# Performance work log

Measured on AMD Instinct MI355X. Metric: run time of the kernel, lower is better.

The kernel has to match this reference:

```python
import jax, jax.numpy as jnp
import numpy as np

N, E, D, L, G, T = 50000, 600000, 128, 4, 512, 10
EPS = 1e-5


def setup_inputs() -> dict:
    key = jax.random.key(0)
    ks = jax.random.split(key, 20)
    s = lambda k, shp, fan: jax.random.normal(k, shp, jnp.float32) * (1.0 / np.sqrt(fan))
    inp = {
        'x': jax.random.normal(ks[0], (N, 3), jnp.float32),
        'edge_index': jax.random.randint(ks[1], (2, E), 0, N, jnp.int32),
        'batch': jnp.sort(jax.random.randint(ks[2], (N,), 0, G, jnp.int32)),
        'emb_W': s(ks[3], (3, D), 3),
        'emb_b': jnp.zeros((D,), jnp.float32),
        'conv_W': s(ks[4], (L, 12 * D, D), 12 * D),
        'conv_b': jnp.zeros((L, D), jnp.float32),
        'bn_gamma': jnp.ones((L, D), jnp.float32),
        'bn_beta': jnp.zeros((L, D), jnp.float32),
        'W1': s(ks[5], (D, D // 2), D), 'b1': jnp.zeros((D // 2,), jnp.float32),
        'W2': s(ks[6], (D // 2, D // 4), D // 2), 'b2': jnp.zeros((D // 4,), jnp.float32),
        'W3': s(ks[7], (D // 4, T), D // 4), 'b3': jnp.zeros((T,), jnp.float32),
    }
    return inp


def reference(x, edge_index, batch, emb_W, emb_b, conv_W, conv_b, bn_gamma, bn_beta,
              W1, b1, W2, b2, W3, b3):
    n = x.shape[0]
    src, dst = edge_index[0], edge_index[1]  # messages flow src(j) -> dst(i)
    deg = jax.ops.segment_sum(jnp.ones((src.shape[0],), x.dtype), dst, num_segments=n)
    delta = jnp.mean(jnp.log1p(deg))          # avg log-degree (PNA's avg_deg['log'])
    d = jnp.maximum(deg, 1.0)[:, None]        # clamp(min=1)
    log_d = jnp.log1p(d)
    amp, att = log_d / delta, delta / log_d   # amplification / attenuation scalers
    has_edge = (deg > 0)[:, None]

    h = x @ emb_W + emb_b                     # node_emb Linear(3, D)
    for l in range(conv_W.shape[0]):
        msg = h[src]                          # [E, D] gather
        s1 = jax.ops.segment_sum(msg, dst, num_segments=n)
        s2 = jax.ops.segment_sum(msg * msg, dst, num_segments=n)
        mean = s1 / d
        std = jnp.sqrt(jax.nn.relu(s2 / d - mean * mean) + EPS)
        mn = jnp.where(has_edge, jax.ops.segment_min(msg, dst, num_segments=n), 0.0)
        mx = jnp.where(has_edge, jax.ops.segment_max(msg, dst, num_segments=n), 0.0)
        aggs = jnp.concatenate([mean, mn, mx, std], axis=-1)                 # [N, 4D]
        out = jnp.concatenate([aggs, aggs * amp, aggs * att], axis=-1)       # [N, 12D]
        out = out @ conv_W[l] + conv_b[l]      # post_nn Linear(12D, D)
        mu = out.mean(axis=0)
        var = out.var(axis=0)
        out = (out - mu) * jax.lax.rsqrt(var + EPS) * bn_gamma[l] + bn_beta[l]
        h = jax.nn.relu(out) + h               # residual (dropout off: eval)

    # global_mean_pool over graphs
    gsum = jax.ops.segment_sum(h, batch, num_segments=G)
    cnt = jnp.maximum(jax.ops.segment_sum(jnp.ones((n,), h.dtype), batch, num_segments=G), 1.0)
    g = gsum / cnt[:, None]
    g = jax.nn.relu(g @ W1 + b1)
    g = jax.nn.relu(g @ W2 + b2)
    return g @ W3 + b3                         # source='image': no clamp
```

## Files before the change

kernel.cpp:

```cpp
#include <hip/hip_runtime.h>
#include <math.h>

#define NN 50000
#define NE 600000
#define DD 128
#define NL 4
#define NG 512
#define NT 10
#define NPAD 50176
#define EPSF 1e-5f

typedef __bf16 bf16x8 __attribute__((ext_vector_type(8)));
typedef float f32x4 __attribute__((ext_vector_type(4)));

__device__ __forceinline__ unsigned short f2bf(float x) {
    union { float f; unsigned u; } v; v.f = x;
    unsigned r = v.u + 0x7FFFu + ((v.u >> 16) & 1u);
    return (unsigned short)(r >> 16);
}
__device__ __forceinline__ unsigned pack_bf2(float a, float b) {
    return (unsigned)f2bf(a) | ((unsigned)f2bf(b) << 16);
}
__device__ __forceinline__ float bf_lo(unsigned v) {
    union { unsigned u; float f; } w; w.u = (v & 0xFFFFu) << 16; return w.f;
}
__device__ __forceinline__ float bf_hi(unsigned v) {
    union { unsigned u; float f; } w; w.u = v & 0xFFFF0000u; return w.f;
}

__global__ void k_count(const int* __restrict__ dst, int* __restrict__ deg,
                        float* __restrict__ dsum, int E) {
    int e = blockIdx.x * blockDim.x + threadIdx.x;
    if (e == 0) *dsum = 0.f;
    if (e < E) atomicAdd(&deg[dst[e]], 1);
}

__global__ void k_scan_part(const int* __restrict__ deg, int* __restrict__ part, int n) {
    __shared__ int sm[256];
    int b = blockIdx.x, t = threadIdx.x;
    int base = b * 1024 + t * 4;
    int s = 0;
    #pragma unroll
    for (int j = 0; j < 4; j++) if (base + j < n) s += deg[base + j];
    sm[t] = s;
    __syncthreads();
    for (int off = 128; off > 0; off >>= 1) {
        if (t < off) sm[t] += sm[t + off];
        __syncthreads();
    }
    if (t == 0) part[b] = sm[0];
}

__global__ void k_scan_top(const int* __restrict__ part, int* __restrict__ offs,
                           int* __restrict__ row_ptr, int nb, int n) {
    if (threadIdx.x == 0) {
        int acc = 0;
        for (int i = 0; i < nb; i++) { offs[i] = acc; acc += part[i]; }
        row_ptr[n] = acc;
    }
}

__global__ void k_scan_apply(const int* __restrict__ deg, const int* __restrict__ offs,
                             int* __restrict__ row_ptr, int* __restrict__ cursor, int n) {
    __shared__ int sm[256];
    int b = blockIdx.x, t = threadIdx.x;
    int base = b * 1024 + t * 4;
    int v[4]; int s = 0;
    #pragma unroll
    for (int j = 0; j < 4; j++) { v[j] = (base + j < n) ? deg[base + j] : 0; s += v[j]; }
    sm[t] = s;
    __syncthreads();
    for (int off = 1; off < 256; off <<= 1) {
        int y = (t >= off) ? sm[t - off] : 0;
        __syncthreads();
        sm[t] += y;
        __syncthreads();
    }
    int run = offs[b] + sm[t] - s;
    #pragma unroll
    for (int j = 0; j < 4; j++) {
        if (base + j < n) { row_ptr[base + j] = run; cursor[base + j] = run; run += v[j]; }
    }
}

__global__ void k_fill(const int* __restrict__ src, const int* __restrict__ dst,
                       int* __restrict__ cursor, int* __restrict__ csr_src, int E) {
    int e = blockIdx.x * blockDim.x + threadIdx.x;
    if (e < E) {
        int d = dst[e];
        int pos = atomicAdd(&cursor[d], 1);
        csr_src[pos] = src[e];
    }
}

__global__ void k_delta(const int* __restrict__ deg, float* __restrict__ dsum, int n) {
    int i = blockIdx.x * blockDim.x + threadIdx.x;
    float v = (i < n) ? log1pf((float)deg[i]) : 0.f;
    #pragma unroll
    for (int off = 32; off > 0; off >>= 1) v += __shfl_down(v, off);
    if ((threadIdx.x & 63) == 0) atomicAdd(dsum, v);
}

__global__ void k_scalars(const int* __restrict__ deg, const float* __restrict__ dsum,
                          float* __restrict__ inv_d, float* __restrict__ amp,
                          float* __restrict__ att, int n) {
    int i = blockIdx.x * blockDim.x + threadIdx.x;
    if (i >= n) return;
    float delta = *dsum / (float)n;
    float d = fmaxf((float)deg[i], 1.f);
    float ld = log1pf(d);
    inv_d[i] = 1.f / d;
    amp[i] = ld / delta;
    att[i] = delta / ld;
}

__global__ void k_emb(const float* __restrict__ x, const float* __restrict__ W,
                      const float* __restrict__ b, float* __restrict__ h,
                      unsigned* __restrict__ hb2, int total2) {
    int i = blockIdx.x * blockDim.x + threadIdx.x;
    if (i >= total2) return;
    int node = i >> 6, c = (i & 63) * 2;
    float x0 = x[node * 3 + 0], x1 = x[node * 3 + 1], x2 = x[node * 3 + 2];
    float v0 = x0 * W[c] + x1 * W[DD + c] + x2 * W[2 * DD + c] + b[c];
    float v1 = x0 * W[c + 1] + x1 * W[DD + c + 1] + x2 * W[2 * DD + c + 1] + b[c + 1];
    ((float2*)h)[i] = make_float2(v0, v1);
    hb2[i] = pack_bf2(v0, v1);
}

__global__ void k_wconv(const float* __restrict__ W, unsigned short* __restrict__ Bt2, int total) {
    int o = blockIdx.x * blockDim.x + threadIdx.x;
    if (o >= total) return;
    int l = o / 196608;
    int idx = o % 196608;
    int kc = idx / 3072;
    int rem = idx % 3072;
    int j = rem >> 10;
    int nn = (rem >> 3) & 127;
    int k8 = rem & 7;
    int k = kc * 8 + k8;
    Bt2[o] = f2bf(W[(size_t)l * 196608 + (size_t)(j * 512 + k) * 128 + nn]);
}

__global__ void k_agg(const unsigned* __restrict__ hb2, const int* __restrict__ row_ptr,
                      const int* __restrict__ csr_src, const float* __restrict__ inv_d,
                      unsigned* __restrict__ atw, float* __restrict__ bn_zero) {
    __shared__ unsigned ldsb[16 * 260];
    int tid = threadIdx.x;
    if (blockIdx.x == 0) bn_zero[tid] = 0.f;
    int w = tid >> 6, t = tid & 63;
    int node0 = blockIdx.x * 16;
    #pragma unroll 1
    for (int q = 0; q < 4; q++) {
        int nl = w * 4 + q;
        int node = node0 + nl;
        int beg = row_ptr[node], end = row_ptr[node + 1];
        float s1a = 0.f, s1b = 0.f, s2a = 0.f, s2b = 0.f;
        float mna = INFINITY, mnb = INFINITY, mxa = -INFINITY, mxb = -INFINITY;
        int e = beg;
        for (; e + 1 < end; e += 2) {
            int sa = csr_src[e], sb = csr_src[e + 1];
            unsigned va = hb2[(size_t)sa * 64 + t];
            unsigned vb = hb2[(size_t)sb * 64 + t];
            float a0 = bf_lo(va), b0 = bf_hi(va);
            float a1 = bf_lo(vb), b1 = bf_hi(vb);
            s1a += a0 + a1; s2a += a0 * a0 + a1 * a1;
            mna = fminf(mna, fminf(a0, a1)); mxa = fmaxf(mxa, fmaxf(a0, a1));
            s1b += b0 + b1; s2b += b0 * b0 + b1 * b1;
            mnb = fminf(mnb, fminf(b0, b1)); mxb = fmaxf(mxb, fmaxf(b0, b1));
        }
        if (e < end) {
            int sa = csr_src[e];
            unsigned va = hb2[(size_t)sa * 64 + t];
            float a0 = bf_lo(va), b0 = bf_hi(va);
            s1a += a0; s2a += a0 * a0; mna = fminf(mna, a0); mxa = fmaxf(mxa, a0);
            s1b += b0; s2b += b0 * b0; mnb = fminf(mnb, b0); mxb = fmaxf(mxb, b0);
        }
        float id = inv_d[node];
        float meana = s1a * id, meanb = s1b * id;
        float sda = sqrtf(fmaxf(s2a * id - meana * meana, 0.f) + EPSF);
        float sdb = sqrtf(fmaxf(s2b * id - meanb * meanb, 0.f) + EPSF);
        if (beg == end) { mna = 0.f; mxa = 0.f; mnb = 0.f; mxb = 0.f; }
        int base = nl * 260;
        ldsb[base + 0 * 64 + t] = pack_bf2(meana, meanb);
        ldsb[base + 1 * 64 + t] = pack_bf2(mna, mnb);
        ldsb[base + 2 * 64 + t] = pack_bf2(mxa, mxb);
        ldsb[base + 3 * 64 + t] = pack_bf2(sda, sdb);
    }
    __syncthreads();
    #pragma unroll
    for (int p = 0; p < 4; p++) {
        int id = p * 256 + tid;
        int node = id & 15, c = id >> 4;
        int sec = c >> 4, cb = c & 15;
        const unsigned* s = &ldsb[node * 260 + sec * 64 + cb * 4];
        uint4 v = make_uint4(s[0], s[1], s[2], s[3]);
        *(uint4*)&atw[((size_t)c * NPAD + node0 + node) * 4] = v;
    }
}

__global__ __launch_bounds__(256, 2) void k_gemm_mfma(
    const unsigned short* __restrict__ At, const unsigned short* __restrict__ Bt2,
    const float* __restrict__ bias, const float* __restrict__ amp,
    const float* __restrict__ att, float* __restrict__ outp,
    float* __restrict__ bn_sum, float* __restrict__ bn_sq, int n) {
    int tid = threadIdx.x;
    int w = tid >> 6, lane = tid & 63;
    int quad = lane >> 4, l16 = lane & 15;
    int bid = blockIdx.x;
    int tile = (bid >> 5) * 8 + (bid & 7);
    int cg = (bid >> 3) & 3;
    if (tile >= 196) return;
    int c0 = cg * 32;
    int base = tile * 256 + w * 64;

    f32x4 acc[4][2][3];
    #pragma unroll
    for (int rt = 0; rt < 4; rt++)
        #pragma unroll
        for (int ct = 0; ct < 2; ct++)
            #pragma unroll
            for (int j = 0; j < 3; j++) acc[rt][ct][j] = (f32x4)(0.f);

    const unsigned short* pA = At + ((size_t)quad * NPAD + base + l16) * 8;
    const unsigned short* pB = Bt2 + ((size_t)quad * 384 + c0 + l16) * 8;
    const size_t stepA = (size_t)4 * NPAD * 8;
    const int stepB = 4 * 384 * 8;

    bf16x8 af0[4], af1[4], bf0[2][3], bf1[2][3];
    auto loadA = [&](bf16x8* dst) {
        #pragma unroll
        for (int rt = 0; rt < 4; rt++) dst[rt] = *(const bf16x8*)(pA + rt * 128);
        pA += stepA;
    };
    auto loadB = [&](bf16x8 (*dst)[3]) {
        #pragma unroll
        for (int ct = 0; ct < 2; ct++)
            #pragma unroll
            for (int j = 0; j < 3; j++)
                dst[ct][j] = *(const bf16x8*)(pB + j * 1024 + ct * 128);
        pB += stepB;
    };
    auto domfma = [&](bf16x8* af, bf16x8 (*bf)[3]) {
        #pragma unroll
        for (int ct = 0; ct < 2; ct++)
            #pragma unroll
            for (int j = 0; j < 3; j++)
                #pragma unroll
                for (int rt = 0; rt < 4; rt++)
                    acc[rt][ct][j] = __builtin_amdgcn_mfma_f32_16x16x32_bf16(
                        af[rt], bf[ct][j], acc[rt][ct][j], 0, 0, 0);
    };

    loadA(af0); loadB(bf0);
    #pragma unroll 1
    for (int it = 0; it < 16; it += 2) {
        loadA(af1); loadB(bf1);
        domfma(af0, bf0);
        loadA(af0); loadB(bf0);
        domfma(af1, bf1);
    }

    float psum[2] = {0.f, 0.f}, psq[2] = {0.f, 0.f};
    #pragma unroll
    for (int rt = 0; rt < 4; rt++) {
        #pragma unroll
        for (int reg = 0; reg < 4; reg++) {
            int row = base + rt * 16 + quad * 4 + reg;
            if (row < n) {
                float am = amp[row], at = att[row];
                #pragma unroll
                for (int ct = 0; ct < 2; ct++) {
                    int col = c0 + ct * 16 + l16;
                    float v = acc[rt][ct][0][reg] + am * acc[rt][ct][1][reg]
                            + at * acc[rt][ct][2][reg] + bias[col];
                    outp[(size_t)row * DD + col] = v;
                    psum[ct] += v;
                    psq[ct] += v * v;
                }
            }
        }
    }
    #pragma unroll
    for (int ct = 0; ct < 2; ct++) {
        psum[ct] += __shfl_xor(psum[ct], 16, 64);
        psum[ct] += __shfl_xor(psum[ct], 32, 64);
        psq[ct]  += __shfl_xor(psq[ct], 16, 64);
        psq[ct]  += __shfl_xor(psq[ct], 32, 64);
    }
    if (quad == 0) {
        #pragma unroll
        for (int ct = 0; ct < 2; ct++) {
            int col = c0 + ct * 16 + l16;
            atomicAdd(&bn_sum[col], psum[ct]);
            atomicAdd(&bn_sq[col], psq[ct]);
        }
    }
}

__global__ void k_bnapply(const float* __restrict__ outp, const float* __restrict__ bn_sum,
                          const float* __restrict__ bn_sq, const float* __restrict__ gamma,
                          const float* __restrict__ beta, float* __restrict__ h,
                          unsigned* __restrict__ hb2, int total4) {
    int i = blockIdx.x * blockDim.x + threadIdx.x;
    if (i >= total4) return;
    int c = (i & 31) * 4;
    const float invn = 1.f / (float)NN;
    float4 o = ((const float4*)outp)[i];
    float4 hh = ((float4*)h)[i];
    float oo[4] = {o.x, o.y, o.z, o.w};
    float hs[4] = {hh.x, hh.y, hh.z, hh.w};
    #pragma unroll
    for (int j = 0; j < 4; j++) {
        float mu = bn_sum[c + j] * invn;
        float var = bn_sq[c + j] * invn - mu * mu;
        float sc = rsqrtf(var + EPSF) * gamma[c + j];
        float sh = beta[c + j] - mu * sc;
        hs[j] += fmaxf(oo[j] * sc + sh, 0.f);
    }
    ((float4*)h)[i] = make_float4(hs[0], hs[1], hs[2], hs[3]);
    hb2[i * 2]     = pack_bf2(hs[0], hs[1]);
    hb2[i * 2 + 1] = pack_bf2(hs[2], hs[3]);
}

__global__ void k_pool_mlp(const float* __restrict__ h, const int* __restrict__ batch,
                           const float* __restrict__ W1, const float* __restrict__ b1,
                           const float* __restrict__ W2, const float* __restrict__ b2,
                           const float* __restrict__ W3, const float* __restrict__ b3,
                           float* __restrict__ out, int n) {
    __shared__ float gvec[128];
    __shared__ float h1[64];
    __shared__ float h2[32];
    __shared__ int srange[2];
    int g = blockIdx.x;
    int t = threadIdx.x;
    if (t < 2) {
        int target = g + t;
        int lo = 0, hi = n;
        while (lo < hi) {
            int mid = (lo + hi) >> 1;
            if (batch[mid] < target) lo = mid + 1; else hi = mid;
        }
        srange[t] = lo;
    }
    __syncthreads();
    int s = srange[0], e = srange[1];
    float acc = 0.f;
    for (int i = s; i < e; i++) acc += h[(size_t)i * DD + t];
    float cnt = fmaxf((float)(e - s), 1.f);
    gvec[t] = acc / cnt;
    __syncthreads();
    if (t < 64) {
        float a = b1[t];
        for (int k = 0; k < 128; k++) a += gvec[k] * W1[k * 64 + t];
        h1[t] = fmaxf(a, 0.f);
    }
    __syncthreads();
    if (t < 32) {
        float a = b2[t];
        for (int k = 0; k < 64; k++) a += h1[k] * W2[k * 32 + t];
        h2[t] = fmaxf(a, 0.f);
    }
    __syncthreads();
    if (t < 10) {
        float a = b3[t];
        for (int k = 0; k < 32; k++) a += h2[k] * W3[k * 10 + t];
        out[g * NT + t] = a;
    }
}

extern "C" void kernel_launch(void* const* d_in, const int* in_sizes, int n_in,
                              void* d_out, int out_size, void* d_ws, size_t ws_size,
                              hipStream_t stream) {
    const float* x      = (const float*)d_in[0];
    const int*   eidx   = (const int*)d_in[1];
    const int*   batch  = (const int*)d_in[2];
    const float* emb_W  = (const float*)d_in[3];
    const float* emb_b  = (const float*)d_in[4];
    const float* conv_W = (const float*)d_in[5];
    const float* conv_b = (const float*)d_in[6];
    const float* bn_g   = (const float*)d_in[7];
    const float* bn_b   = (const float*)d_in[8];
    const float* W1 = (const float*)d_in[9];
    const float* b1 = (const float*)d_in[10];
    const float* W2 = (const float*)d_in[11];
    const float* b2 = (const float*)d_in[12];
    const float* W3 = (const float*)d_in[13];
    const float* b3 = (const float*)d_in[14];
    float* out = (float*)d_out;

    const int* src = eidx;
    const int* dst = eidx + NE;

    char* p = (char*)d_ws;
    auto carve = [&](size_t bytes) {
        void* r = (void*)p;
        p += (bytes + 255) & ~(size_t)255;
        return r;
    };
    int* deg      = (int*)carve(NN * 4);
    int* row_ptr  = (int*)carve((NN + 1) * 4);
    int* cursor   = (int*)carve(NN * 4);
    int* csr_src  = (int*)carve(NE * 4);
    int* part     = (int*)carve(64 * 4);
    int* offs     = (int*)carve(64 * 4);
    float* inv_d  = (float*)carve(NN * 4);
    float* amp    = (float*)carve(NN * 4);
    float* att    = (float*)carve(NN * 4);
    float* dsum   = (float*)carve(4);
    float* bn_sum = (float*)carve(DD * 4);
    float* bn_sq  = (float*)carve(DD * 4);
    float* h      = (float*)carve((size_t)NN * DD * 4);
    unsigned* hb2 = (unsigned*)carve((size_t)NN * 64 * 4);
    unsigned* At  = (unsigned*)carve((size_t)68 * NPAD * 16);
    float* outp   = (float*)carve((size_t)NN * DD * 4);
    unsigned short* Bt2 = (unsigned short*)carve(((size_t)NL * 196608 + 12288) * 2);

    hipMemsetAsync(deg, 0, NN * 4, stream);

    const int NSB = (NN + 1023) / 1024;
    k_count<<<(NE + 255) / 256, 256, 0, stream>>>(dst, deg, dsum, NE);
    k_scan_part<<<NSB, 256, 0, stream>>>(deg, part, NN);
    k_scan_top<<<1, 64, 0, stream>>>(part, offs, row_ptr, NSB, NN);
    k_scan_apply<<<NSB, 256, 0, stream>>>(deg, offs, row_ptr, cursor, NN);
    k_fill<<<(NE + 255) / 256, 256, 0, stream>>>(src, dst, cursor, csr_src, NE);
    k_delta<<<(NN + 255) / 256, 256, 0, stream>>>(deg, dsum, NN);
    k_scalars<<<(NN + 255) / 256, 256, 0, stream>>>(deg, dsum, inv_d, amp, att, NN);
    k_emb<<<(NN * 64 + 255) / 256, 256, 0, stream>>>(x, emb_W, emb_b, h, hb2, NN * 64);
    k_wconv<<<(NL * 196608 + 255) / 256, 256, 0, stream>>>(conv_W, Bt2, NL * 196608);

    const int gemm_blocks = 800;
    for (int l = 0; l < NL; l++) {
        k_agg<<<NN / 16, 256, 0, stream>>>(hb2, row_ptr, csr_src, inv_d, At, bn_sum);
        k_gemm_mfma<<<gemm_blocks, 256, 0, stream>>>(
            (const unsigned short*)At, Bt2 + (size_t)l * 196608,
            conv_b + l * DD, amp, att, outp, bn_sum, bn_sq, NN);
        k_bnapply<<<(NN * 32 + 255) / 256, 256, 0, stream>>>(
            outp, bn_sum, bn_sq, bn_g + l * DD, bn_b + l * DD, h, hb2, NN * 32);
    }

    k_pool_mlp<<<NG, 128, 0, stream>>>(h, batch, W1, b1, W2, b2, W3, b3, out, NN);
}
```

Before: 678.6 us.

## Drop fp32 residual state, keep node features only in bf16; unroll gather by 4

Removes the fp32 copy of node features h. The residual update, the embedding and the mean pool now read and write only the packed bf16 buffer, which cuts memory traffic in the batch-norm apply kernel and the pool kernel. The aggregation loop is unrolled to four edges per iteration so more gathers are in flight at once. The cost is that the residual stream now accumulates in bf16 across layers, which adds rounding error to the output.

```diff
diff --git a/kernel.cpp b/kernel.cpp
--- a/kernel.cpp
+++ b/kernel.cpp
@@ -115,15 +115,13 @@
 }
 
 __global__ void k_emb(const float* __restrict__ x, const float* __restrict__ W,
-                      const float* __restrict__ b, float* __restrict__ h,
-                      unsigned* __restrict__ hb2, int total2) {
+                      const float* __restrict__ b, unsigned* __restrict__ hb2, int total2) {
     int i = blockIdx.x * blockDim.x + threadIdx.x;
     if (i >= total2) return;
     int node = i >> 6, c = (i & 63) * 2;
     float x0 = x[node * 3 + 0], x1 = x[node * 3 + 1], x2 = x[node * 3 + 2];
     float v0 = x0 * W[c] + x1 * W[DD + c] + x2 * W[2 * DD + c] + b[c];
     float v1 = x0 * W[c + 1] + x1 * W[DD + c + 1] + x2 * W[2 * DD + c + 1] + b[c + 1];
-    ((float2*)h)[i] = make_float2(v0, v1);
     hb2[i] = pack_bf2(v0, v1);
 }
 
@@ -157,18 +155,27 @@
         float s1a = 0.f, s1b = 0.f, s2a = 0.f, s2b = 0.f;
         float mna = INFINITY, mnb = INFINITY, mxa = -INFINITY, mxb = -INFINITY;
         int e = beg;
-        for (; e + 1 < end; e += 2) {
-            int sa = csr_src[e], sb = csr_src[e + 1];
+        for (; e + 3 < end; e += 4) {
+            int sa = csr_src[e],     sb = csr_src[e + 1];
+            int sc = csr_src[e + 2], sd = csr_src[e + 3];
             unsigned va = hb2[(size_t)sa * 64 + t];
             unsigned vb = hb2[(size_t)sb * 64 + t];
+            unsigned vc = hb2[(size_t)sc * 64 + t];
+            unsigned vd = hb2[(size_t)sd * 64 + t];
             float a0 = bf_lo(va), b0 = bf_hi(va);
             float a1 = bf_lo(vb), b1 = bf_hi(vb);
-            s1a += a0 + a1; s2a += a0 * a0 + a1 * a1;
-            mna = fminf(mna, fminf(a0, a1)); mxa = fmaxf(mxa, fmaxf(a0, a1));
-            s1b += b0 + b1; s2b += b0 * b0 + b1 * b1;
-            mnb = fminf(mnb, fminf(b0, b1)); mxb = fmaxf(mxb, fmaxf(b0, b1));
+            float a2 = bf_lo(vc), b2 = bf_hi(vc);
+            float a3 = bf_lo(vd), b3 = bf_hi(vd);
+            s1a += (a0 + a1) + (a2 + a3);
+            s2a += a0 * a0 + a1 * a1 + a2 * a2 + a3 * a3;
+            mna = fminf(fminf(mna, fminf(a0, a1)), fminf(a2, a3));
+            mxa = fmaxf(fmaxf(mxa, fmaxf(a0, a1)), fmaxf(a2, a3));
+            s1b += (b0 + b1) + (b2 + b3);
+            s2b += b0 * b0 + b1 * b1 + b2 * b2 + b3 * b3;
+            mnb = fminf(fminf(mnb, fminf(b0, b1)), fminf(b2, b3));
+            mxb = fmaxf(fmaxf(mxb, fmaxf(b0, b1)), fmaxf(b2, b3));
         }
-        if (e < end) {
+        for (; e < end; e++) {
             int sa = csr_src[e];
             unsigned va = hb2[(size_t)sa * 64 + t];
             float a0 = bf_lo(va), b0 = bf_hi(va);
@@ -299,30 +306,37 @@
 
 __global__ void k_bnapply(const float* __restrict__ outp, const float* __restrict__ bn_sum,
                           const float* __restrict__ bn_sq, const float* __restrict__ gamma,
-                          const float* __restrict__ beta, float* __restrict__ h,
-                          unsigned* __restrict__ hb2, int total4) {
+                          const float* __restrict__ beta, unsigned* __restrict__ hb2,
+                          int total8) {
     int i = blockIdx.x * blockDim.x + threadIdx.x;
-    if (i >= total4) return;
-    int c = (i & 31) * 4;
+    if (i >= total8) return;
+    int c = (i & 15) * 8;
     const float invn = 1.f / (float)NN;
-    float4 o = ((const float4*)outp)[i];
-    float4 hh = ((float4*)h)[i];
-    float oo[4] = {o.x, o.y, o.z, o.w};
-    float hs[4] = {hh.x, hh.y, hh.z, hh.w};
-    #pragma unroll
-    for (int j = 0; j < 4; j++) {
-        float mu = bn_sum[c + j] * invn;
-        float var = bn_sq[c + j] * invn - mu * mu;
-        float sc = rsqrtf(var + EPSF) * gamma[c + j];
-        float sh = beta[c + j] - mu * sc;
-        hs[j] += fmaxf(oo[j] * sc + sh, 0.f);
-    }
-    ((float4*)h)[i] = make_float4(hs[0], hs[1], hs[2], hs[3]);
-    hb2[i * 2]     = pack_bf2(hs[0], hs[1]);
-    hb2[i * 2 + 1] = pack_bf2(hs[2], hs[3]);
-}
-
-__global__ void k_pool_mlp(const float* __restrict__ h, const int* __restrict__ batch,
+    float4 o0 = ((const float4*)outp)[i * 2];
+    float4 o1 = ((const float4*)outp)[i * 2 + 1];
+    uint4 hv = ((const uint4*)hb2)[i];
+    float oo[8] = {o0.x, o0.y, o0.z, o0.w, o1.x, o1.y, o1.z, o1.w};
+    unsigned hu[4] = {hv.x, hv.y, hv.z, hv.w};
+    unsigned ru[4];
+    #pragma unroll
+    for (int p = 0; p < 4; p++) {
+        int c0 = c + p * 2;
+        float mu0 = bn_sum[c0] * invn;
+        float var0 = bn_sq[c0] * invn - mu0 * mu0;
+        float sc0 = rsqrtf(var0 + EPSF) * gamma[c0];
+        float sh0 = beta[c0] - mu0 * sc0;
+        float mu1 = bn_sum[c0 + 1] * invn;
+        float var1 = bn_sq[c0 + 1] * invn - mu1 * mu1;
+        float sc1 = rsqrtf(var1 + EPSF) * gamma[c0 + 1];
+        float sh1 = beta[c0 + 1] - mu1 * sc1;
+        float v0 = fmaxf(oo[p * 2] * sc0 + sh0, 0.f) + bf_lo(hu[p]);
+        float v1 = fmaxf(oo[p * 2 + 1] * sc1 + sh1, 0.f) + bf_hi(hu[p]);
+        ru[p] = pack_bf2(v0, v1);
+    }
+    ((uint4*)hb2)[i] = make_uint4(ru[0], ru[1], ru[2], ru[3]);
+}
+
+__global__ void k_pool_mlp(const unsigned* __restrict__ hb2, const int* __restrict__ batch,
                            const float* __restrict__ W1, const float* __restrict__ b1,
                            const float* __restrict__ W2, const float* __restrict__ b2,
                            const float* __restrict__ W3, const float* __restrict__ b3,
@@ -344,8 +358,12 @@
     }
     __syncthreads();
     int s = srange[0], e = srange[1];
+    int p = t >> 1, odd = t & 1;
     float acc = 0.f;
-    for (int i = s; i < e; i++) acc += h[(size_t)i * DD + t];
+    for (int i = s; i < e; i++) {
+        unsigned v = hb2[(size_t)i * 64 + p];
+        acc += odd ? bf_hi(v) : bf_lo(v);
+    }
     float cnt = fmaxf((float)(e - s), 1.f);
     gvec[t] = acc / cnt;
     __syncthreads();
@@ -409,7 +427,6 @@
     float* dsum   = (float*)carve(4);
     float* bn_sum = (float*)carve(DD * 4);
     float* bn_sq  = (float*)carve(DD * 4);
-    float* h      = (float*)carve((size_t)NN * DD * 4);
     unsigned* hb2 = (unsigned*)carve((size_t)NN * 64 * 4);
     unsigned* At  = (unsigned*)carve((size_t)68 * NPAD * 16);
     float* outp   = (float*)carve((size_t)NN * DD * 4);
@@ -425,7 +442,7 @@
     k_fill<<<(NE + 255) / 256, 256, 0, stream>>>(src, dst, cursor, csr_src, NE);
     k_delta<<<(NN + 255) / 256, 256, 0, stream>>>(deg, dsum, NN);
     k_scalars<<<(NN + 255) / 256, 256, 0, stream>>>(deg, dsum, inv_d, amp, att, NN);
-    k_emb<<<(NN * 64 + 255) / 256, 256, 0, stream>>>(x, emb_W, emb_b, h, hb2, NN * 64);
+    k_emb<<<(NN * 64 + 255) / 256, 256, 0, stream>>>(x, emb_W, emb_b, hb2, NN * 64);
     k_wconv<<<(NL * 196608 + 255) / 256, 256, 0, stream>>>(conv_W, Bt2, NL * 196608);
 
     const int gemm_blocks = 800;
@@ -434,9 +451,9 @@
         k_gemm_mfma<<<gemm_blocks, 256, 0, stream>>>(
             (const unsigned short*)At, Bt2 + (size_t)l * 196608,
             conv_b + l * DD, amp, att, outp, bn_sum, bn_sq, NN);
-        k_bnapply<<<(NN * 32 + 255) / 256, 256, 0, stream>>>(
-            outp, bn_sum, bn_sq, bn_g + l * DD, bn_b + l * DD, h, hb2, NN * 32);
-    }
-
-    k_pool_mlp<<<NG, 128, 0, stream>>>(h, batch, W1, b1, W2, b2, W3, b3, out, NN);
-}
+        k_bnapply<<<(NN * 16 + 255) / 256, 256, 0, stream>>>(
+            outp, bn_sum, bn_sq, bn_g + l * DD, bn_b + l * DD, hb2, NN * 16);
+    }
+
+    k_pool_mlp<<<NG, 128, 0, stream>>>(hb2, batch, W1, b1, W2, b2, W3, b3, out, NN);
+}
```

After: 616.9 us. 9.1% less time.
